# Kernel tuning notes

Measured on AMD Instinct MI355X. Metric: run time of the kernel, lower is better.

Reference implementation:

```python
import jax, jax.numpy as jnp
import numpy as np

N = 200000   # atoms
M = 12       # neighbors per atom
F = 64       # atom_fea_len
NBR = 41     # nbr_fea_len
ORIG = 92    # orig_atom_fea_len
B = 2000     # crystals
SH = 9       # dim of 0e+1o+2e spherical harmonics (lmax=2)
NCONV = 3
HFEA = 128


def _sph_harm_l2(v):
    # real spherical harmonics up to l=2 on normalized vectors ('integral' norm)
    r = jnp.sqrt(jnp.sum(v * v, axis=-1, keepdims=True))
    u = v / jnp.maximum(r, 1e-9)
    x, y, z = u[..., 0], u[..., 1], u[..., 2]
    c0 = 0.28209479177387814   # 1/(2*sqrt(pi))
    c1 = 0.4886025119029199    # sqrt(3/(4*pi))
    c2 = 1.0925484305920792
    return jnp.stack([
        jnp.full_like(x, c0),
        c1 * y, c1 * z, c1 * x,
        c2 * x * y, c2 * y * z,
        0.31539156525252005 * (3.0 * z * z - 1.0),
        c2 * x * z,
        0.5462742152960396 * (x * x - y * y),
    ], axis=-1)


def setup_inputs() -> dict:
    key = jax.random.key(0)
    ks = jax.random.split(key, 12)
    s = 0.05
    return {
        "atom_fea": jax.random.normal(ks[0], (N, ORIG), jnp.float32),
        "nbr_fea": jax.random.uniform(ks[1], (N, M, NBR), dtype=jnp.float32),
        "nbr_idx": jax.random.randint(ks[2], (N, M), 0, N),
        "crystal_atom_idx": jnp.arange(N).reshape(B, N // B),
        "pos": jax.random.normal(ks[3], (N, 3), jnp.float32),
        "W_emb": jax.random.normal(ks[4], (ORIG, F), jnp.float32) * s,
        "b_emb": jnp.zeros((F,), jnp.float32),
        "Wr1": jax.random.normal(ks[5], (NCONV, NBR, NBR), jnp.float32) * s,
        "br1": jnp.zeros((NCONV, NBR), jnp.float32),
        "Wr2": jax.random.normal(ks[6], (NCONV, NBR, SH), jnp.float32) * s,
        "br2": jnp.zeros((NCONV, SH), jnp.float32),
        "Wtp": jax.random.normal(ks[7], (NCONV, F, F), jnp.float32) * s,
        "W_fc": jax.random.normal(ks[8], (F, HFEA), jnp.float32) * s,
        "b_fc": jnp.zeros((HFEA,), jnp.float32),
        "W_out": jax.random.normal(ks[9], (HFEA, 1), jnp.float32) * s,
        "b_out": jnp.zeros((1,), jnp.float32),
    }


def reference(atom_fea, nbr_fea, nbr_idx, crystal_atom_idx, pos,
              W_emb, b_emb, Wr1, br1, Wr2, br2, Wtp, W_fc, b_fc, W_out, b_out):
    x = atom_fea @ W_emb + b_emb                       # [N, F]
    src = nbr_idx.reshape(-1)                          # [N*M]
    e = nbr_fea.reshape(N * M, NBR)
    # dst = arange(N) repeated M times -> pos[dst] is just pos repeated
    rel = pos[src] - jnp.repeat(pos, M, axis=0)        # [N*M, 3]
    Y = _sph_harm_l2(rel)                              # [N*M, 9]
    Y0 = Y[:, :1]                                      # only 0e path feeds the TP output
    alpha = 1.0 / jnp.sqrt(jnp.float32(F))             # e3nn path normalization
    for l in range(NCONV):
        R = jax.nn.softplus(e @ Wr1[l] + br1[l]) @ Wr2[l] + br2[l]   # [N*M, 9]
        W0 = R[:, :1] * Y0                                           # scalar gate per edge
        msg = (x[src] @ Wtp[l]) * W0 * alpha                          # [N*M, F]
        # scatter-mean over dst == mean over the fixed M neighbors
        x = msg.reshape(N, M, F).mean(axis=1)
    crys = x[crystal_atom_idx].mean(axis=1)            # [B, F]
    h = jax.nn.softplus(crys @ W_fc + b_fc)            # [B, HFEA]
    out = h @ W_out + b_out                            # [B, 1]
    return (out, h)
```

## Files before the change

### kernel.cpp

```cpp
#include <hip/hip_runtime.h>
#include <hip/hip_bf16.h>
#include <math.h>

#define N_ATOMS 200000
#define M_NBR 12
#define F_DIM 64
#define NBR_FEA 41
#define ORIG_F 92
#define B_CRYS 2000
#define APB 100
#define SH_DIM 9
#define NCONV 3
#define HFEA 128
#define EDGES (N_ATOMS * M_NBR)

typedef __attribute__((ext_vector_type(8))) short short8;
typedef __attribute__((ext_vector_type(4))) float floatx4;

struct f4u { float x, y, z, w; };

__device__ __forceinline__ unsigned short f2bf(float f) {
    __hip_bfloat16 h = __float2bfloat16(f);
    return *reinterpret_cast<unsigned short*>(&h);
}
__device__ __forceinline__ float bf2f(unsigned int u) {
    unsigned int x = u << 16;
    union { unsigned int i; float f; } c; c.i = x; return c.f;
}
__device__ __forceinline__ float softplus_f(float x) {
    return fmaxf(x, 0.0f) + __logf(1.0f + __expf(-fabsf(x)));
}

__global__ __launch_bounds__(256) void k_embed(
    const float* __restrict__ atom_fea, const float* __restrict__ W_emb,
    const float* __restrict__ b_emb, unsigned short* __restrict__ x)
{
    __shared__ float ldsW[ORIG_F * F_DIM];
    __shared__ float ldsA[16 * ORIG_F];
    int tid = threadIdx.x;
    for (int i = tid; i < ORIG_F * F_DIM; i += 256) ldsW[i] = W_emb[i];
    long base = (long)blockIdx.x * 16;
    for (int i = tid; i < 16 * ORIG_F; i += 256) ldsA[i] = atom_fea[base * ORIG_F + i];
    __syncthreads();
    int col = tid & 63;
    int rg  = tid >> 6;
    float a0 = 0.f, a1 = 0.f, a2 = 0.f, a3 = 0.f;
    const float* Ar = &ldsA[(rg * 4) * ORIG_F];
    for (int k = 0; k < ORIG_F; ++k) {
        float wv = ldsW[k * F_DIM + col];
        a0 = fmaf(Ar[0 * ORIG_F + k], wv, a0);
        a1 = fmaf(Ar[1 * ORIG_F + k], wv, a1);
        a2 = fmaf(Ar[2 * ORIG_F + k], wv, a2);
        a3 = fmaf(Ar[3 * ORIG_F + k], wv, a3);
    }
    float bb = b_emb[col];
    long o = (base + rg * 4) * F_DIM + col;
    x[o]             = f2bf(a0 + bb);
    x[o + F_DIM]     = f2bf(a1 + bb);
    x[o + 2 * F_DIM] = f2bf(a2 + bb);
    x[o + 3 * F_DIM] = f2bf(a3 + bb);
}

__global__ __launch_bounds__(256) void k_prep(
    const float* __restrict__ Wr1, const float* __restrict__ br1,
    const float* __restrict__ Wr2, const float* __restrict__ Wtp,
    unsigned short* __restrict__ wpak, float* __restrict__ w2pk,
    float* __restrict__ b1pk, unsigned short* __restrict__ wtpak)
{
    int t = threadIdx.x;
    for (int i = t; i < 64 * 18 * 8; i += 256) {
        int lane = i / 144;
        int rem  = i - lane * 144;
        int fid  = rem >> 3;
        int j    = rem & 7;
        int l  = fid / 6;
        int rf = fid - l * 6;
        int nt = rf >> 1;
        int s  = rf & 1;
        int n = nt * 16 + (lane & 15);
        int k = s * 32 + (lane >> 4) * 8 + j;
        unsigned short v = 0;
        if (n < NBR_FEA && k < NBR_FEA)
            v = f2bf(Wr1[(l * NBR_FEA + k) * NBR_FEA + n]);
        wpak[i] = v;
    }
    for (int i = t; i < 3 * 64 * 3 * 4; i += 256) {
        int reg = i & 3;
        int q   = i >> 2;
        int nt  = q % 3;
        int q2  = q / 3;
        int lane = q2 & 63;
        int l    = q2 >> 6;
        int n = nt * 16 + (lane >> 4) * 4 + reg;
        float b = 0.f, w = 0.f;
        if (n < NBR_FEA) {
            b = br1[l * NBR_FEA + n];
            w = Wr2[(l * NBR_FEA + n) * SH_DIM];
        }
        b1pk[i] = b;
        w2pk[i] = w;
    }
    for (int i = t; i < 3 * 64 * 64; i += 256) {
        int j = i & 7;
        int q = i >> 3;
        int s = q & 1;  q >>= 1;
        int nt = q & 3; q >>= 2;
        int lane = q & 63;
        int l    = q >> 6;
        int k = s * 32 + (lane >> 4) * 8 + j;
        int n = nt * 16 + (lane & 15);
        wtpak[i] = f2bf(Wtp[(l * F_DIM + k) * F_DIM + n]);
    }
}

__global__ __launch_bounds__(256) void k_filter(
    const float* __restrict__ nbr_fea,
    const unsigned short* __restrict__ wpak,
    const float* __restrict__ w2pk, const float* __restrict__ b1pk,
    const float* __restrict__ br2, float* __restrict__ W0)
{
    int tid  = threadIdx.x;
    int lane = tid & 63;
    int wv   = tid >> 6;
    int sub  = lane & 15;
    int quad = lane >> 4;
    long ebase = (long)blockIdx.x * 256;

    short8 efr[4][2];
    #pragma unroll
    for (int mt = 0; mt < 4; ++mt) {
        long r = ebase + wv * 64 + mt * 16 + sub;
        const float* rowp = nbr_fea + r * NBR_FEA;
        f4u a = *(const f4u*)(rowp + quad * 8);
        f4u b = *(const f4u*)(rowp + quad * 8 + 4);
        short8 f0;
        f0[0] = (short)f2bf(a.x); f0[1] = (short)f2bf(a.y);
        f0[2] = (short)f2bf(a.z); f0[3] = (short)f2bf(a.w);
        f0[4] = (short)f2bf(b.x); f0[5] = (short)f2bf(b.y);
        f0[6] = (short)f2bf(b.z); f0[7] = (short)f2bf(b.w);
        efr[mt][0] = f0;
        short8 f1 = {0, 0, 0, 0, 0, 0, 0, 0};
        if (quad == 0) {
            f4u c = *(const f4u*)(rowp + 32);
            f4u d = *(const f4u*)(rowp + 36);
            f1[0] = (short)f2bf(c.x); f1[1] = (short)f2bf(c.y);
            f1[2] = (short)f2bf(c.z); f1[3] = (short)f2bf(c.w);
            f1[4] = (short)f2bf(d.x); f1[5] = (short)f2bf(d.y);
            f1[6] = (short)f2bf(d.z); f1[7] = (short)f2bf(d.w);
        } else if (quad == 1) {
            f1[0] = (short)f2bf(rowp[40]);
        }
        efr[mt][1] = f1;
    }

    const unsigned short* abase = wpak + lane * 144;

    #pragma unroll
    for (int l = 0; l < NCONV; ++l) {
        short8 wfr[3][2];
        #pragma unroll
        for (int nt = 0; nt < 3; ++nt)
            #pragma unroll
            for (int s = 0; s < 2; ++s)
                wfr[nt][s] = *(const short8*)(abase + ((l * 3 + nt) * 2 + s) * 8);

        floatx4 b1v[3], w2v[3], w2l[3];
        #pragma unroll
        for (int nt = 0; nt < 3; ++nt) {
            b1v[nt] = *(const floatx4*)&b1pk[((l * 64 + lane) * 3 + nt) * 4];
            w2v[nt] = *(const floatx4*)&w2pk[((l * 64 + lane) * 3 + nt) * 4];
            w2l[nt] = w2v[nt] * 0.69314718055994531f;
        }

        floatx4 acc[3][4];
        #pragma unroll
        for (int nt = 0; nt < 3; ++nt)
            #pragma unroll
            for (int mt = 0; mt < 4; ++mt)
                acc[nt][mt] = b1v[nt];

        #pragma unroll
        for (int s = 0; s < 2; ++s)
            #pragma unroll
            for (int nt = 0; nt < 3; ++nt)
                #pragma unroll
                for (int mt = 0; mt < 4; ++mt)
                    acc[nt][mt] = __builtin_amdgcn_mfma_f32_16x16x32_bf16(
                        wfr[nt][s], efr[mt][s], acc[nt][mt], 0, 0, 0);

        float r2b = br2[l * SH_DIM];
        #pragma unroll
        for (int mt = 0; mt < 4; ++mt) {
            float t = 0.f;
            #pragma unroll
            for (int nt = 0; nt < 3; ++nt)
                #pragma unroll
                for (int reg = 0; reg < 4; ++reg) {
                    float x  = acc[nt][mt][reg];
                    float e  = __expf(-fabsf(x));
                    float lg = __log2f(1.0f + e);
                    t = fmaf(fmaxf(x, 0.f), w2v[nt][reg], fmaf(lg, w2l[nt][reg], t));
                }
            t += __shfl_xor(t, 16);
            t += __shfl_xor(t, 32);
            if (quad == 0)
                W0[(long)l * EDGES + ebase + wv * 64 + mt * 16 + sub] = t + r2b;
        }
    }
}

__global__ __launch_bounds__(256) void k_conv(
    const unsigned short* __restrict__ x_in, const int* __restrict__ nbr_idx,
    const float* __restrict__ W0, const unsigned short* __restrict__ wtp,
    unsigned short* __restrict__ x_out)
{
    __shared__ __align__(16) unsigned short gl[32 * F_DIM];
    int tid  = threadIdx.x;
    int lane = tid & 63;
    int wv   = tid >> 6;
    int aw   = lane >> 3;
    int oct  = lane & 7;
    const float cscale = 0.28209479177387814f * 0.125f / 12.0f;

    int  al   = wv * 8 + aw;
    long atom = (long)blockIdx.x * 32 + al;
    long eb   = atom * M_NBR;
    float a0=0.f,a1=0.f,a2=0.f,a3=0.f,a4=0.f,a5=0.f,a6=0.f,a7=0.f;
    #pragma unroll
    for (int j = 0; j < M_NBR; ++j) {
        int   idx = nbr_idx[eb + j];
        float wj  = W0[eb + j];
        uint4 v = *(const uint4*)(x_in + (size_t)idx * F_DIM + oct * 8);
        a0 = fmaf(wj, bf2f(v.x & 0xffffu), a0);
        a1 = fmaf(wj, bf2f(v.x >> 16),     a1);
        a2 = fmaf(wj, bf2f(v.y & 0xffffu), a2);
        a3 = fmaf(wj, bf2f(v.y >> 16),     a3);
        a4 = fmaf(wj, bf2f(v.z & 0xffffu), a4);
        a5 = fmaf(wj, bf2f(v.z >> 16),     a5);
        a6 = fmaf(wj, bf2f(v.w & 0xffffu), a6);
        a7 = fmaf(wj, bf2f(v.w >> 16),     a7);
    }
    short8 pk;
    pk[0] = (short)f2bf(a0 * cscale); pk[1] = (short)f2bf(a1 * cscale);
    pk[2] = (short)f2bf(a2 * cscale); pk[3] = (short)f2bf(a3 * cscale);
    pk[4] = (short)f2bf(a4 * cscale); pk[5] = (short)f2bf(a5 * cscale);
    pk[6] = (short)f2bf(a6 * cscale); pk[7] = (short)f2bf(a7 * cscale);
    int wb = (al * 128 + oct * 16) ^ ((al & 7) << 4);
    *(short8*)((char*)gl + wb) = pk;
    __syncthreads();

    int sub = lane & 15, quad = lane >> 4;
    int mt = wv & 1;
    int nb = (wv >> 1) * 2;
    short8 afr[2];
    #pragma unroll
    for (int s = 0; s < 2; ++s) {
        int row = mt * 16 + sub;
        int rb = (row * 128 + s * 64 + quad * 16) ^ ((row & 7) << 4);
        afr[s] = *(const short8*)((const char*)gl + rb);
    }
    const unsigned short* bb = wtp + lane * 64;
    floatx4 acc[2] = {{0.f,0.f,0.f,0.f},{0.f,0.f,0.f,0.f}};
    #pragma unroll
    for (int s = 0; s < 2; ++s)
        #pragma unroll
        for (int nti = 0; nti < 2; ++nti) {
            short8 bfr = *(const short8*)(bb + (nb + nti) * 16 + s * 8);
            acc[nti] = __builtin_amdgcn_mfma_f32_16x16x32_bf16(afr[s], bfr, acc[nti], 0, 0, 0);
        }
    size_t ob = ((size_t)blockIdx.x * 32 + mt * 16 + quad * 4) * F_DIM + nb * 16 + sub;
    #pragma unroll
    for (int nti = 0; nti < 2; ++nti)
        #pragma unroll
        for (int reg = 0; reg < 4; ++reg)
            x_out[ob + (size_t)reg * F_DIM + nti * 16] = f2bf(acc[nti][reg]);
}

__global__ __launch_bounds__(128) void k_readout(
    const unsigned short* __restrict__ x, const int* __restrict__ cidx,
    const float* __restrict__ W_fc, const float* __restrict__ b_fc,
    const float* __restrict__ W_out, const float* __restrict__ b_out,
    float* __restrict__ out, float* __restrict__ hout)
{
    __shared__ float part[2][F_DIM];
    __shared__ float crys[F_DIM];
    __shared__ float hw[HFEA];
    int tid = threadIdx.x;
    int c = blockIdx.x;
    int f = tid & 63, half = tid >> 6;
    const int* ci = cidx + c * APB + half * (APB / 2);
    float p = 0.f;
    for (int a = 0; a < APB / 2; ++a)
        p += bf2f(x[(size_t)ci[a] * F_DIM + f]);
    part[half][f] = p;
    __syncthreads();
    if (tid < F_DIM) crys[tid] = (part[0][tid] + part[1][tid]) * (1.0f / APB);
    __syncthreads();
    float acc = b_fc[tid];
    for (int ff = 0; ff < F_DIM; ++ff)
        acc = fmaf(crys[ff], W_fc[ff * HFEA + tid], acc);
    float h = softplus_f(acc);
    hout[(size_t)c * HFEA + tid] = h;
    hw[tid] = h * W_out[tid];
    __syncthreads();
    if (tid == 0) {
        float s = b_out[0];
        #pragma unroll 16
        for (int j = 0; j < HFEA; ++j) s += hw[j];
        out[c] = s;
    }
}

extern "C" void kernel_launch(void* const* d_in, const int* in_sizes, int n_in,
                              void* d_out, int out_size, void* d_ws, size_t ws_size,
                              hipStream_t stream) {
    const float* atom_fea = (const float*)d_in[0];
    const float* nbr_fea  = (const float*)d_in[1];
    const int*   nbr_idx  = (const int*)d_in[2];
    const int*   cidx     = (const int*)d_in[3];
    const float* W_emb = (const float*)d_in[5];
    const float* b_emb = (const float*)d_in[6];
    const float* Wr1   = (const float*)d_in[7];
    const float* br1   = (const float*)d_in[8];
    const float* Wr2   = (const float*)d_in[9];
    const float* br2   = (const float*)d_in[10];
    const float* Wtp   = (const float*)d_in[11];
    const float* W_fc  = (const float*)d_in[12];
    const float* b_fc  = (const float*)d_in[13];
    const float* W_out = (const float*)d_in[14];
    const float* b_out = (const float*)d_in[15];

    float* out  = (float*)d_out;
    float* hout = out + B_CRYS;

    float* W0 = (float*)d_ws;
    unsigned short* xA = (unsigned short*)(W0 + 3 * (size_t)EDGES);
    unsigned short* xB = xA + (size_t)N_ATOMS * F_DIM;

    unsigned short* wpak = xB;
    float* w2pk = (float*)(wpak + 9216);
    float* b1pk = w2pk + 2304;
    unsigned short* wtpak = (unsigned short*)(hout + 128000);

    k_prep  <<<1, 256, 0, stream>>>(Wr1, br1, Wr2, Wtp, wpak, w2pk, b1pk, wtpak);
    k_embed <<<N_ATOMS / 16, 256, 0, stream>>>(atom_fea, W_emb, b_emb, xA);
    k_filter<<<EDGES / 256, 256, 0, stream>>>(nbr_fea, wpak, w2pk, b1pk, br2, W0);
    k_conv  <<<N_ATOMS / 32, 256, 0, stream>>>(xA, nbr_idx, W0,             wtpak,            xB);
    k_conv  <<<N_ATOMS / 32, 256, 0, stream>>>(xB, nbr_idx, W0 + EDGES,     wtpak + 4096,     xA);
    k_conv  <<<N_ATOMS / 32, 256, 0, stream>>>(xA, nbr_idx, W0 + 2 * EDGES, wtpak + 2 * 4096, xB);
    k_readout<<<B_CRYS, 128, 0, stream>>>(xB, cidx, W_fc, b_fc, W_out, b_out, out, hout);
}
```

Baseline: 923.6 us.

## Use MFMA for embedding, fold log2 scaling into filter weights, vectorise conv and readout

```diff
diff --git a/kernel.cpp b/kernel.cpp
--- a/kernel.cpp
+++ b/kernel.cpp
@@ -27,46 +27,24 @@
     unsigned int x = u << 16;
     union { unsigned int i; float f; } c; c.i = x; return c.f;
 }
+__device__ __forceinline__ unsigned int pk2(float lo, float hi) {
+    return (unsigned int)f2bf(lo) | ((unsigned int)f2bf(hi) << 16);
+}
 __device__ __forceinline__ float softplus_f(float x) {
     return fmaxf(x, 0.0f) + __logf(1.0f + __expf(-fabsf(x)));
 }
 
-__global__ __launch_bounds__(256) void k_embed(
-    const float* __restrict__ atom_fea, const float* __restrict__ W_emb,
-    const float* __restrict__ b_emb, unsigned short* __restrict__ x)
-{
-    __shared__ float ldsW[ORIG_F * F_DIM];
-    __shared__ float ldsA[16 * ORIG_F];
-    int tid = threadIdx.x;
-    for (int i = tid; i < ORIG_F * F_DIM; i += 256) ldsW[i] = W_emb[i];
-    long base = (long)blockIdx.x * 16;
-    for (int i = tid; i < 16 * ORIG_F; i += 256) ldsA[i] = atom_fea[base * ORIG_F + i];
-    __syncthreads();
-    int col = tid & 63;
-    int rg  = tid >> 6;
-    float a0 = 0.f, a1 = 0.f, a2 = 0.f, a3 = 0.f;
-    const float* Ar = &ldsA[(rg * 4) * ORIG_F];
-    for (int k = 0; k < ORIG_F; ++k) {
-        float wv = ldsW[k * F_DIM + col];
-        a0 = fmaf(Ar[0 * ORIG_F + k], wv, a0);
-        a1 = fmaf(Ar[1 * ORIG_F + k], wv, a1);
-        a2 = fmaf(Ar[2 * ORIG_F + k], wv, a2);
-        a3 = fmaf(Ar[3 * ORIG_F + k], wv, a3);
-    }
-    float bb = b_emb[col];
-    long o = (base + rg * 4) * F_DIM + col;
-    x[o]             = f2bf(a0 + bb);
-    x[o + F_DIM]     = f2bf(a1 + bb);
-    x[o + 2 * F_DIM] = f2bf(a2 + bb);
-    x[o + 3 * F_DIM] = f2bf(a3 + bb);
-}
 
 __global__ __launch_bounds__(256) void k_prep(
     const float* __restrict__ Wr1, const float* __restrict__ br1,
     const float* __restrict__ Wr2, const float* __restrict__ Wtp,
+    const float* __restrict__ W_emb, const float* __restrict__ b_emb,
     unsigned short* __restrict__ wpak, float* __restrict__ w2pk,
-    float* __restrict__ b1pk, unsigned short* __restrict__ wtpak)
+    float* __restrict__ b1pk, unsigned short* __restrict__ wtpak,
+    unsigned short* __restrict__ wepak, float* __restrict__ bepk)
 {
+    const float LOG2E = 1.4426950408889634f;
+    const float LN2   = 0.69314718055994531f;
     int t = threadIdx.x;
     for (int i = t; i < 64 * 18 * 8; i += 256) {
         int lane = i / 144;
@@ -81,7 +59,7 @@
         int k = s * 32 + (lane >> 4) * 8 + j;
         unsigned short v = 0;
         if (n < NBR_FEA && k < NBR_FEA)
-            v = f2bf(Wr1[(l * NBR_FEA + k) * NBR_FEA + n]);
+            v = f2bf(Wr1[(l * NBR_FEA + k) * NBR_FEA + n] * LOG2E);
         wpak[i] = v;
     }
     for (int i = t; i < 3 * 64 * 3 * 4; i += 256) {
@@ -94,8 +72,8 @@
         int n = nt * 16 + (lane >> 4) * 4 + reg;
         float b = 0.f, w = 0.f;
         if (n < NBR_FEA) {
-            b = br1[l * NBR_FEA + n];
-            w = Wr2[(l * NBR_FEA + n) * SH_DIM];
+            b = br1[l * NBR_FEA + n] * LOG2E;
+            w = Wr2[(l * NBR_FEA + n) * SH_DIM] * LN2;
         }
         b1pk[i] = b;
         w2pk[i] = w;
@@ -110,6 +88,71 @@
         int k = s * 32 + (lane >> 4) * 8 + j;
         int n = nt * 16 + (lane & 15);
         wtpak[i] = f2bf(Wtp[(l * F_DIM + k) * F_DIM + n]);
+    }
+    for (int i = t; i < 64 * 12 * 8; i += 256) {
+        int j = i & 7;
+        int q = i >> 3;
+        int s = q % 3;
+        int q2 = q / 3;
+        int nt = q2 & 3;
+        int lane = q2 >> 2;
+        int n = nt * 16 + (lane & 15);
+        int k = s * 32 + (lane >> 4) * 8 + j;
+        wepak[i] = (k < ORIG_F) ? f2bf(W_emb[k * F_DIM + n]) : (unsigned short)0;
+    }
+    for (int i = t; i < 64 * 4 * 4; i += 256) {
+        int reg = i & 3;
+        int q = i >> 2;
+        int nt = q & 3;
+        int lane = q >> 2;
+        bepk[i] = b_emb[nt * 16 + (lane >> 4) * 4 + reg];
+    }
+}
+
+__global__ __launch_bounds__(256) void k_embed(
+    const float* __restrict__ atom_fea, const unsigned short* __restrict__ wepak,
+    const float* __restrict__ bepk, unsigned short* __restrict__ x)
+{
+    int tid  = threadIdx.x;
+    int lane = tid & 63;
+    int wv   = tid >> 6;
+    int sub  = lane & 15;
+    int quad = lane >> 4;
+    long arow = (long)blockIdx.x * 64 + wv * 16 + sub;
+    const float* ap = atom_fea + arow * ORIG_F;
+
+    short8 bfrg[3];
+    #pragma unroll
+    for (int s = 0; s < 3; ++s) {
+        int ko = s * 32 + quad * 8;
+        short8 f = {0,0,0,0,0,0,0,0};
+        f4u a = *(const f4u*)(ap + ko);
+        f[0] = (short)f2bf(a.x); f[1] = (short)f2bf(a.y);
+        f[2] = (short)f2bf(a.z); f[3] = (short)f2bf(a.w);
+        if (s < 2 || quad < 3) {
+            f4u b = *(const f4u*)(ap + ko + 4);
+            f[4] = (short)f2bf(b.x); f[5] = (short)f2bf(b.y);
+            f[6] = (short)f2bf(b.z); f[7] = (short)f2bf(b.w);
+        }
+        bfrg[s] = f;
+    }
+
+    const unsigned short* wb = wepak + lane * 96;
+    floatx4 acc[4];
+    #pragma unroll
+    for (int nt = 0; nt < 4; ++nt)
+        acc[nt] = *(const floatx4*)&bepk[(lane * 4 + nt) * 4];
+    #pragma unroll
+    for (int s = 0; s < 3; ++s)
+        #pragma unroll
+        for (int nt = 0; nt < 4; ++nt)
+            acc[nt] = __builtin_amdgcn_mfma_f32_16x16x32_bf16(
+                *(const short8*)(wb + (nt * 3 + s) * 8), bfrg[s], acc[nt], 0, 0, 0);
+
+    #pragma unroll
+    for (int nt = 0; nt < 4; ++nt) {
+        uint2 o = { pk2(acc[nt][0], acc[nt][1]), pk2(acc[nt][2], acc[nt][3]) };
+        *(uint2*)&x[arow * F_DIM + nt * 16 + quad * 4] = o;
     }
 }
 
@@ -164,12 +207,11 @@
             for (int s = 0; s < 2; ++s)
                 wfr[nt][s] = *(const short8*)(abase + ((l * 3 + nt) * 2 + s) * 8);
 
-        floatx4 b1v[3], w2v[3], w2l[3];
+        floatx4 b1v[3], w2v[3];
         #pragma unroll
         for (int nt = 0; nt < 3; ++nt) {
             b1v[nt] = *(const floatx4*)&b1pk[((l * 64 + lane) * 3 + nt) * 4];
             w2v[nt] = *(const floatx4*)&w2pk[((l * 64 + lane) * 3 + nt) * 4];
-            w2l[nt] = w2v[nt] * 0.69314718055994531f;
         }
 
         floatx4 acc[3][4];
@@ -196,10 +238,10 @@
             for (int nt = 0; nt < 3; ++nt)
                 #pragma unroll
                 for (int reg = 0; reg < 4; ++reg) {
-                    float x  = acc[nt][mt][reg];
-                    float e  = __expf(-fabsf(x));
+                    float xv = acc[nt][mt][reg];
+                    float e  = exp2f(-fabsf(xv));
                     float lg = __log2f(1.0f + e);
-                    t = fmaf(fmaxf(x, 0.f), w2v[nt][reg], fmaf(lg, w2l[nt][reg], t));
+                    t = fmaf(fmaxf(xv, 0.f) + lg, w2v[nt][reg], t);
                 }
             t += __shfl_xor(t, 16);
             t += __shfl_xor(t, 32);
@@ -214,6 +256,8 @@
     const float* __restrict__ W0, const unsigned short* __restrict__ wtp,
     unsigned short* __restrict__ x_out)
 {
+    __shared__ int   sIdx[32 * M_NBR];
+    __shared__ float sW  [32 * M_NBR];
     __shared__ __align__(16) unsigned short gl[32 * F_DIM];
     int tid  = threadIdx.x;
     int lane = tid & 63;
@@ -221,25 +265,39 @@
     int aw   = lane >> 3;
     int oct  = lane & 7;
     const float cscale = 0.28209479177387814f * 0.125f / 12.0f;
-
-    int  al   = wv * 8 + aw;
-    long atom = (long)blockIdx.x * 32 + al;
-    long eb   = atom * M_NBR;
+    long abase = (long)blockIdx.x * 32;
+
+    if (tid < 96)
+        ((int4*)sIdx)[tid] = ((const int4*)(nbr_idx + abase * M_NBR))[tid];
+    else if (tid < 192)
+        ((float4*)sW)[tid - 96] = ((const float4*)(W0 + abase * M_NBR))[tid - 96];
+    __syncthreads();
+
+    int al = wv * 8 + aw;
+    int4   i0 = *(const int4*)&sIdx[al * M_NBR];
+    int4   i1 = *(const int4*)&sIdx[al * M_NBR + 4];
+    int4   i2 = *(const int4*)&sIdx[al * M_NBR + 8];
+    float4 w0 = *(const float4*)&sW[al * M_NBR];
+    float4 w1 = *(const float4*)&sW[al * M_NBR + 4];
+    float4 w2 = *(const float4*)&sW[al * M_NBR + 8];
+
+    const unsigned short* xb = x_in + oct * 8;
     float a0=0.f,a1=0.f,a2=0.f,a3=0.f,a4=0.f,a5=0.f,a6=0.f,a7=0.f;
-    #pragma unroll
-    for (int j = 0; j < M_NBR; ++j) {
-        int   idx = nbr_idx[eb + j];
-        float wj  = W0[eb + j];
-        uint4 v = *(const uint4*)(x_in + (size_t)idx * F_DIM + oct * 8);
-        a0 = fmaf(wj, bf2f(v.x & 0xffffu), a0);
-        a1 = fmaf(wj, bf2f(v.x >> 16),     a1);
-        a2 = fmaf(wj, bf2f(v.y & 0xffffu), a2);
-        a3 = fmaf(wj, bf2f(v.y >> 16),     a3);
-        a4 = fmaf(wj, bf2f(v.z & 0xffffu), a4);
-        a5 = fmaf(wj, bf2f(v.z >> 16),     a5);
-        a6 = fmaf(wj, bf2f(v.w & 0xffffu), a6);
-        a7 = fmaf(wj, bf2f(v.w >> 16),     a7);
-    }
+    #define GJ(IDX, WW) { \
+        uint4 v = *(const uint4*)(xb + (size_t)(IDX) * F_DIM); \
+        a0 = fmaf(WW, bf2f(v.x & 0xffffu), a0); \
+        a1 = fmaf(WW, bf2f(v.x >> 16),     a1); \
+        a2 = fmaf(WW, bf2f(v.y & 0xffffu), a2); \
+        a3 = fmaf(WW, bf2f(v.y >> 16),     a3); \
+        a4 = fmaf(WW, bf2f(v.z & 0xffffu), a4); \
+        a5 = fmaf(WW, bf2f(v.z >> 16),     a5); \
+        a6 = fmaf(WW, bf2f(v.w & 0xffffu), a6); \
+        a7 = fmaf(WW, bf2f(v.w >> 16),     a7); }
+    GJ(i0.x, w0.x) GJ(i0.y, w0.y) GJ(i0.z, w0.z) GJ(i0.w, w0.w)
+    GJ(i1.x, w1.x) GJ(i1.y, w1.y) GJ(i1.z, w1.z) GJ(i1.w, w1.w)
+    GJ(i2.x, w2.x) GJ(i2.y, w2.y) GJ(i2.z, w2.z) GJ(i2.w, w2.w)
+    #undef GJ
+
     short8 pk;
     pk[0] = (short)f2bf(a0 * cscale); pk[1] = (short)f2bf(a1 * cscale);
     pk[2] = (short)f2bf(a2 * cscale); pk[3] = (short)f2bf(a3 * cscale);
@@ -250,14 +308,13 @@
     __syncthreads();
 
     int sub = lane & 15, quad = lane >> 4;
-    int mt = wv & 1;
+    int at = (wv & 1) * 16 + sub;
     int nb = (wv >> 1) * 2;
-    short8 afr[2];
+    short8 gfr[2];
     #pragma unroll
     for (int s = 0; s < 2; ++s) {
-        int row = mt * 16 + sub;
-        int rb = (row * 128 + s * 64 + quad * 16) ^ ((row & 7) << 4);
-        afr[s] = *(const short8*)((const char*)gl + rb);
+        int rb = (at * 128 + s * 64 + quad * 16) ^ ((at & 7) << 4);
+        gfr[s] = *(const short8*)((const char*)gl + rb);
     }
     const unsigned short* bb = wtp + lane * 64;
     floatx4 acc[2] = {{0.f,0.f,0.f,0.f},{0.f,0.f,0.f,0.f}};
@@ -265,15 +322,15 @@
     for (int s = 0; s < 2; ++s)
         #pragma unroll
         for (int nti = 0; nti < 2; ++nti) {
-            short8 bfr = *(const short8*)(bb + (nb + nti) * 16 + s * 8);
-            acc[nti] = __builtin_amdgcn_mfma_f32_16x16x32_bf16(afr[s], bfr, acc[nti], 0, 0, 0);
-        }
-    size_t ob = ((size_t)blockIdx.x * 32 + mt * 16 + quad * 4) * F_DIM + nb * 16 + sub;
-    #pragma unroll
-    for (int nti = 0; nti < 2; ++nti)
-        #pragma unroll
-        for (int reg = 0; reg < 4; ++reg)
-            x_out[ob + (size_t)reg * F_DIM + nti * 16] = f2bf(acc[nti][reg]);
+            short8 wfr = *(const short8*)(bb + (nb + nti) * 16 + s * 8);
+            acc[nti] = __builtin_amdgcn_mfma_f32_16x16x32_bf16(wfr, gfr[s], acc[nti], 0, 0, 0);
+        }
+    size_t ob = ((size_t)blockIdx.x * 32 + (wv & 1) * 16 + sub) * F_DIM;
+    #pragma unroll
+    for (int nti = 0; nti < 2; ++nti) {
+        uint2 o = { pk2(acc[nti][0], acc[nti][1]), pk2(acc[nti][2], acc[nti][3]) };
+        *(uint2*)&x_out[ob + (nb + nti) * 16 + quad * 4] = o;
+    }
 }
 
 __global__ __launch_bounds__(128) void k_readout(
@@ -282,24 +339,42 @@
     const float* __restrict__ W_out, const float* __restrict__ b_out,
     float* __restrict__ out, float* __restrict__ hout)
 {
-    __shared__ float part[2][F_DIM];
+    __shared__ int sIdx[APB];
+    __shared__ float4 red[8][16];
     __shared__ float crys[F_DIM];
     __shared__ float hw[HFEA];
     int tid = threadIdx.x;
     int c = blockIdx.x;
-    int f = tid & 63, half = tid >> 6;
-    const int* ci = cidx + c * APB + half * (APB / 2);
-    float p = 0.f;
-    for (int a = 0; a < APB / 2; ++a)
-        p += bf2f(x[(size_t)ci[a] * F_DIM + f]);
-    part[half][f] = p;
-    __syncthreads();
-    if (tid < F_DIM) crys[tid] = (part[0][tid] + part[1][tid]) * (1.0f / APB);
-    __syncthreads();
-    float acc = b_fc[tid];
+    if (tid < APB) sIdx[tid] = cidx[c * APB + tid];
+    __syncthreads();
+    int cq = tid & 15, rg = tid >> 4;
+    float4 acc = {0.f, 0.f, 0.f, 0.f};
+    for (int r = rg; r < APB; r += 8) {
+        int a = sIdx[r];
+        uint2 v = *(const uint2*)(x + (size_t)a * F_DIM + cq * 4);
+        acc.x += bf2f(v.x & 0xffffu);
+        acc.y += bf2f(v.x >> 16);
+        acc.z += bf2f(v.y & 0xffffu);
+        acc.w += bf2f(v.y >> 16);
+    }
+    red[rg][cq] = acc;
+    __syncthreads();
+    if (tid < 16) {
+        float4 s = red[0][tid];
+        #pragma unroll
+        for (int g = 1; g < 8; ++g) {
+            float4 r4 = red[g][tid];
+            s.x += r4.x; s.y += r4.y; s.z += r4.z; s.w += r4.w;
+        }
+        const float inv = 1.0f / APB;
+        s.x *= inv; s.y *= inv; s.z *= inv; s.w *= inv;
+        *(float4*)&crys[tid * 4] = s;
+    }
+    __syncthreads();
+    float acc2 = b_fc[tid];
     for (int ff = 0; ff < F_DIM; ++ff)
-        acc = fmaf(crys[ff], W_fc[ff * HFEA + tid], acc);
-    float h = softplus_f(acc);
+        acc2 = fmaf(crys[ff], W_fc[ff * HFEA + tid], acc2);
+    float h = softplus_f(acc2);
     hout[(size_t)c * HFEA + tid] = h;
     hw[tid] = h * W_out[tid];
     __syncthreads();
@@ -337,13 +412,16 @@
     unsigned short* xA = (unsigned short*)(W0 + 3 * (size_t)EDGES);
     unsigned short* xB = xA + (size_t)N_ATOMS * F_DIM;
 
-    unsigned short* wpak = xB;
-    float* w2pk = (float*)(wpak + 9216);
-    float* b1pk = w2pk + 2304;
+    unsigned short* wpak  = xB;
+    float*          w2pk  = (float*)(wpak + 9216);
+    float*          b1pk  = w2pk + 2304;
+    unsigned short* wepak = (unsigned short*)(b1pk + 2304);
+    float*          bepk  = (float*)(wepak + 6144);
     unsigned short* wtpak = (unsigned short*)(hout + 128000);
 
-    k_prep  <<<1, 256, 0, stream>>>(Wr1, br1, Wr2, Wtp, wpak, w2pk, b1pk, wtpak);
-    k_embed <<<N_ATOMS / 16, 256, 0, stream>>>(atom_fea, W_emb, b_emb, xA);
+    k_prep  <<<1, 256, 0, stream>>>(Wr1, br1, Wr2, Wtp, W_emb, b_emb,
+                                    wpak, w2pk, b1pk, wtpak, wepak, bepk);
+    k_embed <<<N_ATOMS / 64, 256, 0, stream>>>(atom_fea, wepak, bepk, xA);
     k_filter<<<EDGES / 256, 256, 0, stream>>>(nbr_fea, wpak, w2pk, b1pk, br2, W0);
     k_conv  <<<N_ATOMS / 32, 256, 0, stream>>>(xA, nbr_idx, W0,             wtpak,            xB);
     k_conv  <<<N_ATOMS / 32, 256, 0, stream>>>(xB, nbr_idx, W0 + EDGES,     wtpak + 4096,     xA);
```

After: 927.1 us. About the same (+0.4%).
